# Optimization experiments

Hardware: AMD Instinct MI355X
Metric: run time of the kernel (lower is better)

The kernel has to match this reference:

```python
import jax, jax.numpy as jnp
import numpy as np
import math

DIM = 1024
NUM_HEADS = 16
HEAD_DIM = DIM // NUM_HEADS
ROPE_BASE = 10000.0


def _rope_cos_sin(seq_len, head_dim, dtype):
    inv_freq = 1.0 / (ROPE_BASE ** (jnp.arange(0, head_dim, 2, dtype=jnp.float32) / head_dim))
    t = jnp.arange(seq_len, dtype=jnp.float32)
    freqs = jnp.einsum('i,j->ij', t, inv_freq)          # (S, head_dim/2)
    emb = jnp.concatenate([freqs, freqs], axis=-1)      # (S, head_dim)
    return jnp.cos(emb).astype(dtype), jnp.sin(emb).astype(dtype)


def _rotate_half(x):
    x1, x2 = jnp.split(x, 2, axis=-1)
    return jnp.concatenate([-x2, x1], axis=-1)


def setup_inputs() -> dict:
    key = jax.random.key(0)
    kx, kq, kk, kv, ko = jax.random.split(key, 5)
    B, S = 4, 2048
    scale = 1.0 / math.sqrt(DIM)
    x = jax.random.normal(kx, (B, S, DIM), dtype=jnp.float32)
    Wq = jax.random.normal(kq, (DIM, DIM), dtype=jnp.float32) * scale
    Wk = jax.random.normal(kk, (DIM, DIM), dtype=jnp.float32) * scale
    Wv = jax.random.normal(kv, (DIM, DIM), dtype=jnp.float32) * scale
    Wo = jax.random.normal(ko, (DIM, DIM), dtype=jnp.float32) * scale
    mask = jnp.tril(jnp.ones((S, S), dtype=jnp.int32))  # causal mask
    return {"x": x, "Wq": Wq, "Wk": Wk, "Wv": Wv, "Wo": Wo, "mask": mask}


def reference(x, Wq, Wk, Wv, Wo, mask):
    B, S, _ = x.shape
    # projections (nn.Linear: y = x @ W.T)
    def split_heads(t):
        return t.reshape(B, S, NUM_HEADS, HEAD_DIM).transpose(0, 2, 1, 3)  # (B,H,S,D)
    q = split_heads(x @ Wq.T)
    k = split_heads(x @ Wk.T)
    v = split_heads(x @ Wv.T)
    # RoPE
    cos, sin = _rope_cos_sin(S, HEAD_DIM, x.dtype)      # (S, D)
    cos = cos[None, None]; sin = sin[None, None]
    q = q * cos + _rotate_half(q) * sin
    k = k * cos + _rotate_half(k) * sin
    # attention
    scores = jnp.einsum('bhsd,bhtd->bhst', q, k) / math.sqrt(HEAD_DIM)
    neg_inf = jnp.asarray(-jnp.inf, dtype=scores.dtype)
    scores = jnp.where(mask[None, None] == 0, neg_inf, scores)
    attn = jax.nn.softmax(scores, axis=-1)
    out = jnp.einsum('bhst,bhtd->bhsd', attn, v)        # (B,H,S,D)
    out = out.transpose(0, 2, 1, 3).reshape(B, S, DIM)
    return out @ Wo.T
```

## Files before the change

kernel.cpp:

```cpp
#include <hip/hip_runtime.h>
#include <hip/hip_bf16.h>

#define BDIM 1024
#define NH 16
#define HD 64
#define BB 4
#define SS 2048
#define MTOT (BB*SS)
#define NT (SS/64)

typedef __bf16 bf16x8 __attribute__((ext_vector_type(8)));
typedef float f32x4 __attribute__((ext_vector_type(4)));

__device__ __forceinline__ unsigned short f2b(float f){
    __bf16 h = (__bf16)f;
    return __builtin_bit_cast(unsigned short, h);
}

__device__ __forceinline__ void ld16(const unsigned short* g, unsigned short* l){
    __builtin_amdgcn_global_load_lds(
        (const __attribute__((address_space(1))) unsigned int*)(const void*)g,
        (__attribute__((address_space(3))) unsigned int*)(void*)l, 16, 0, 0);
}

__global__ void setup_all(const float* __restrict__ x,
                          const float* __restrict__ Wq, const float* __restrict__ Wk,
                          const float* __restrict__ Wv, const float* __restrict__ Wo,
                          unsigned short* __restrict__ xb,
                          unsigned short* __restrict__ oq, unsigned short* __restrict__ ok,
                          unsigned short* __restrict__ ov, unsigned short* __restrict__ oo,
                          float2* __restrict__ rt){
    const int bid = blockIdx.x;
    const int tid = threadIdx.x;
    if (bid < 8192){
        int i = bid * 256 + tid;
        float4 v = ((const float4*)x)[i];
        ushort4 o;
        o.x = f2b(v.x); o.y = f2b(v.y); o.z = f2b(v.z); o.w = f2b(v.w);
        ((ushort4*)xb)[i] = o;
    } else if (bid < 12288){
        int idx = bid - 8192;
        int which = idx >> 10;
        const float* in = (which == 0) ? Wq : (which == 1) ? Wk : (which == 2) ? Wv : Wo;
        unsigned short* out = (which == 0) ? oq : (which == 1) ? ok : (which == 2) ? ov : oo;
        int i = (idx & 1023) * 256 + tid;
        float4 v = ((const float4*)in)[i];
        ushort4 o;
        o.x = f2b(v.x); o.y = f2b(v.y); o.z = f2b(v.z); o.w = f2b(v.w);
        ((ushort4*)out)[i] = o;
    } else {
        int i = (bid - 12288) * 256 + tid;
        int s = i >> 5, d = i & 31;
        float theta = (float)s * exp2f(-0.41524101186092029f * (float)d);
        float sn, c;
        sincosf(theta, &sn, &c);
        rt[i] = make_float2(c, sn);
    }
}

__device__ __forceinline__ void gemm_mainloop(
    const unsigned short* __restrict__ A,
    const unsigned short* __restrict__ Bw,
    unsigned short* At, unsigned short* Bt,
    f32x4 acc[4][4], int m0, int n0)
{
    const int tid  = threadIdx.x;
    const int lane = tid & 63;
    const int wave = tid >> 6;
    const int wr = wave >> 1, wc = wave & 1;
    const int lh = lane >> 4, ll = lane & 15;
    const int K = 1024;

    for (int k0 = 0; k0 < K; k0 += 64){
        #pragma unroll
        for (int c = 0; c < 4; ++c){
            int g   = c*256 + tid;
            int row = g >> 3;
            int off = (g & 7) * 8;
            int base = (c*256 + wave*64) * 8;
            ld16(A  + (size_t)(m0+row)*K + k0 + off, At + base);
            ld16(Bw + (size_t)(n0+row)*K + k0 + off, Bt + base);
        }
        __syncthreads();
        #pragma unroll
        for (int ks = 0; ks < 2; ++ks){
            bf16x8 af[4], bfr[4];
            #pragma unroll
            for (int i = 0; i < 4; ++i)
                af[i] = *(const bf16x8*)(At + (wr*64 + i*16 + ll)*64 + ks*32 + lh*8);
            #pragma unroll
            for (int j = 0; j < 4; ++j)
                bfr[j] = *(const bf16x8*)(Bt + (wc*64 + j*16 + ll)*64 + ks*32 + lh*8);
            #pragma unroll
            for (int i = 0; i < 4; ++i)
                #pragma unroll
                for (int j = 0; j < 4; ++j)
                    acc[i][j] = __builtin_amdgcn_mfma_f32_16x16x32_bf16(af[i], bfr[j], acc[i][j], 0, 0, 0);
        }
        __syncthreads();
    }
}

#define TILE_US 4096

__global__ __launch_bounds__(256, 4) void gemm_qkv(
    const unsigned short* __restrict__ Xb,
    const unsigned short* __restrict__ Wq,
    const unsigned short* __restrict__ Wk,
    const unsigned short* __restrict__ Wv,
    const float2* __restrict__ Rt,
    unsigned short* __restrict__ Qt,
    unsigned short* __restrict__ Kt,
    unsigned short* __restrict__ VTt)
{
    __shared__ alignas(16) unsigned short At[128*64];
    __shared__ alignas(16) unsigned short Bt[128*64];
    const int z = blockIdx.z;
    const unsigned short* Bw = (z == 0) ? Wq : (z == 1 ? Wk : Wv);
    const int m0 = blockIdx.y * 128, n0 = blockIdx.x * 128;
    f32x4 acc[4][4] = {};
    gemm_mainloop(Xb, Bw, At, Bt, acc, m0, n0);

    const int lane = threadIdx.x & 63;
    const int wave = threadIdx.x >> 6;
    const int wr = wave >> 1, wc = wave & 1;
    const int lh = lane >> 4, ll = lane & 15;
    const int h  = blockIdx.x*2 + wc;
    const int b  = m0 >> 11;
    const int bh = b*NH + h;

    if (z < 2){
        const float qs = (z == 0) ? 0.125f * 1.44269504f : 1.0f;
        unsigned short* C = (z == 0) ? Qt : Kt;
        #pragma unroll
        for (int i = 0; i < 4; ++i)
            #pragma unroll
            for (int r = 0; r < 4; ++r){
                int m = m0 + wr*64 + i*16 + lh*4 + r;
                int s = m & (SS-1);
                int kt = s >> 6;
                const float2* rowcs = Rt + (s << 5);
                size_t fb = ((size_t)(bh*NT + kt)*8 + i)*512 + (size_t)(lh*4 + r)*8;
                #pragma unroll
                for (int jl = 0; jl < 2; ++jl){
                    int d_lo = jl*16 + ll;
                    float2 cs = rowcs[d_lo];
                    float a_lo = acc[i][jl][r], a_hi = acc[i][jl+2][r];
                    float y_lo = (a_lo*cs.x - a_hi*cs.y) * qs;
                    float y_hi = (a_hi*cs.x + a_lo*cs.y) * qs;
                    size_t off = fb + (size_t)(jl*2 + (ll>>3))*128 + (ll&7);
                    C[off]        = f2b(y_lo);
                    C[off + 2048] = f2b(y_hi);
                }
            }
    } else {
        const int s0 = (m0 & (SS-1)) + wr*64;
        const int kt = s0 >> 6;
        #pragma unroll
        for (int i = 0; i < 4; ++i)
            #pragma unroll
            for (int j = 0; j < 4; ++j){
                unsigned short tmp[4];
                #pragma unroll
                for (int r = 0; r < 4; ++r)
                    tmp[r] = f2b(acc[i][j][r]);
                size_t off = ((size_t)(bh*NT + kt)*8 + (i>>1)*4 + j)*512
                           + (size_t)(((i&1)*2 + (lh>>1))*16 + ll)*8 + (lh&1)*4;
                *(uint2*)(VTt + off) = *(const uint2*)tmp;
            }
    }
}

__global__ __launch_bounds__(256, 4) void gemm_out(
    const unsigned short* __restrict__ Ab,
    const unsigned short* __restrict__ Wo,
    float* __restrict__ Cout)
{
    __shared__ alignas(16) unsigned short At[128*64];
    __shared__ alignas(16) unsigned short Bt[128*64];
    const int m0 = blockIdx.y * 128, n0 = blockIdx.x * 128;
    f32x4 acc[4][4] = {};
    gemm_mainloop(Ab, Wo, At, Bt, acc, m0, n0);

    const int lane = threadIdx.x & 63;
    const int wave = threadIdx.x >> 6;
    const int wr = wave >> 1, wc = wave & 1;
    const int lh = lane >> 4, ll = lane & 15;
    #pragma unroll
    for (int i = 0; i < 4; ++i)
        #pragma unroll
        for (int j = 0; j < 4; ++j)
            #pragma unroll
            for (int r = 0; r < 4; ++r){
                int m = m0 + wr*64 + i*16 + lh*4 + r;
                int n = n0 + wc*64 + j*16 + ll;
                Cout[(size_t)m*BDIM + n] = acc[i][j][r];
            }
}

__device__ __forceinline__ void attn_tile(
    const bf16x8 qf[2], bool diag, int ws, int lane, int lh, int ll,
    const unsigned short* Ksh, const unsigned short* Vsh, unsigned short* Prow,
    float li[4], f32x4 o[4])
{
    f32x4 sc[4] = {};
    #pragma unroll
    for (int ks = 0; ks < 2; ++ks)
        #pragma unroll
        for (int j = 0; j < 4; ++j){
            bf16x8 bfr = *(const bf16x8*)(Ksh + (ks*4 + j)*512 + lane*8);
            sc[j] = __builtin_amdgcn_mfma_f32_16x16x32_bf16(qf[ks], bfr, sc[j], 0, 0, 0);
        }
    if (diag){
        #pragma unroll
        for (int j = 0; j < 4; ++j){
            int key = j*16 + ll;
            #pragma unroll
            for (int r = 0; r < 4; ++r){
                int qrow = ws*16 + lh*4 + r;
                if (key > qrow) sc[j][r] = -1e30f;
            }
        }
    }
    #pragma unroll
    for (int j = 0; j < 4; ++j)
        #pragma unroll
        for (int r = 0; r < 4; ++r)
            sc[j][r] = exp2f(sc[j][r] - 28.0f);
    #pragma unroll
    for (int r = 0; r < 4; ++r)
        li[r] += (sc[0][r] + sc[1][r]) + (sc[2][r] + sc[3][r]);
    #pragma unroll
    for (int j = 0; j < 4; ++j)
        #pragma unroll
        for (int r = 0; r < 4; ++r)
            Prow[(lh*4 + r)*72 + j*16 + ll] = f2b(sc[j][r]);
    #pragma unroll
    for (int ks = 0; ks < 2; ++ks){
        bf16x8 pf = *(const bf16x8*)(Prow + ll*72 + ks*32 + lh*8);
        #pragma unroll
        for (int t = 0; t < 4; ++t){
            bf16x8 vf = *(const bf16x8*)(Vsh + (ks*4 + t)*512 + lane*8);
            o[t] = __builtin_amdgcn_mfma_f32_16x16x32_bf16(pf, vf, o[t], 0, 0, 0);
        }
    }
}

__device__ __forceinline__ void store_o(
    unsigned short* S, const f32x4 o[4], const float li[4],
    int lane, int lh, int ll, int q0w, int b, int h,
    unsigned short* __restrict__ Obuf)
{
    #pragma unroll
    for (int r = 0; r < 4; ++r){
        float inv = 1.0f / li[r];
        #pragma unroll
        for (int t = 0; t < 4; ++t)
            S[(lh*4 + r)*72 + t*16 + ll] = f2b(o[t][r] * inv);
    }
    int row = lane >> 2, c4 = (lane & 3) * 8;
    size_t rb = ((size_t)(b*SS + q0w + row))*BDIM + h*HD;
    *(uint4*)(Obuf + rb + c4)      = *(uint4*)(S + row*72 + c4);
    *(uint4*)(Obuf + rb + 32 + c4) = *(uint4*)(S + row*72 + 32 + c4);
}

__global__ __launch_bounds__(512, 4) void attn_kernel(
    const unsigned short* __restrict__ Qt,
    const unsigned short* __restrict__ Kt,
    const unsigned short* __restrict__ VTt,
    unsigned short* __restrict__ Obuf)
{
    __shared__ alignas(16) unsigned short Ksh[2][TILE_US];
    __shared__ alignas(16) unsigned short Vsh[2][TILE_US];
    __shared__ alignas(16) unsigned short Psh[8][16*72];

    const int tid  = threadIdx.x;
    const int lane = tid & 63;
    const int wave = tid >> 6;
    const int grp  = wave >> 2;
    const int ws   = wave & 3;
    const int lh = lane >> 4, ll = lane & 15;
    const int bx = blockIdx.x;
    const int bh = blockIdx.y;

    const int tS = (grp == 0) ? bx        : 15 - bx;
    const int tL = (grp == 0) ? NT-1 - bx : 16 + bx;
    const int ktMax = NT-1 - bx;

    const unsigned short* Qhf = Qt  + (size_t)bh * NT * TILE_US;
    const unsigned short* Khf = Kt  + (size_t)bh * NT * TILE_US;
    const unsigned short* Vhf = VTt + (size_t)bh * NT * TILE_US;

    bf16x8 qfS[2], qfL[2];
    #pragma unroll
    for (int ks = 0; ks < 2; ++ks){
        qfS[ks] = *(const bf16x8*)(Qhf + (size_t)(tS*8 + ks*4 + ws)*512 + lane*8);
        qfL[ks] = *(const bf16x8*)(Qhf + (size_t)(tL*8 + ks*4 + ws)*512 + lane*8);
    }

    f32x4 oS[4] = {}, oL[4] = {};
    float liS[4] = {0.f,0.f,0.f,0.f}, liL[4] = {0.f,0.f,0.f,0.f};

    const int tb = tid * 8;

    {
        uint4 k0 = *(const uint4*)(Khf + tb);
        uint4 v0 = *(const uint4*)(Vhf + tb);
        *(uint4*)(&Ksh[0][0] + tb) = k0;
        *(uint4*)(&Vsh[0][0] + tb) = v0;
    }
    __syncthreads();

    int cur = 0;
    for (int kt = 0; kt <= ktMax; ++kt){
        uint4 kr, vr;
        if (kt < ktMax){
            size_t nb = (size_t)(kt + 1) * TILE_US + tb;
            kr = *(const uint4*)(Khf + nb);
            vr = *(const uint4*)(Vhf + nb);
        }
        if (kt <= tL)
            attn_tile(qfL, kt == tL, ws, lane, lh, ll, &Ksh[cur][0], &Vsh[cur][0], Psh[wave], liL, oL);
        if (kt <= tS)
            attn_tile(qfS, kt == tS, ws, lane, lh, ll, &Ksh[cur][0], &Vsh[cur][0], Psh[wave], liS, oS);
        if (kt < ktMax){
            *(uint4*)(&Ksh[cur^1][0] + tb) = kr;
            *(uint4*)(&Vsh[cur^1][0] + tb) = vr;
        }
        __syncthreads();
        cur ^= 1;
    }

    #pragma unroll
    for (int r = 0; r < 4; ++r){
        float sS = liS[r], sL = liL[r];
        #pragma unroll
        for (int x = 1; x < 16; x <<= 1){
            sS += __shfl_xor(sS, x);
            sL += __shfl_xor(sL, x);
        }
        liS[r] = sS; liL[r] = sL;
    }

    int b = bh >> 4, h = bh & 15;
    store_o(Psh[wave], oS, liS, lane, lh, ll, tS*64 + ws*16, b, h, Obuf);
    store_o(Psh[wave], oL, liL, lane, lh, ll, tL*64 + ws*16, b, h, Obuf);
}

extern "C" void kernel_launch(void* const* d_in, const int* in_sizes, int n_in,
                              void* d_out, int out_size, void* d_ws, size_t ws_size,
                              hipStream_t stream) {
    const float* x  = (const float*)d_in[0];
    const float* Wq = (const float*)d_in[1];
    const float* Wk = (const float*)d_in[2];
    const float* Wv = (const float*)d_in[3];
    const float* Wo = (const float*)d_in[4];

    char* w = (char*)d_ws;
    unsigned short* xb  = (unsigned short*)(w);
    unsigned short* wqb = (unsigned short*)(w + (16u  << 20));
    unsigned short* wkb = (unsigned short*)(w + (18u  << 20));
    unsigned short* wvb = (unsigned short*)(w + (20u  << 20));
    unsigned short* wob = (unsigned short*)(w + (22u  << 20));
    unsigned short* Qt  = (unsigned short*)(w + (24u  << 20));
    unsigned short* Kt  = (unsigned short*)(w + (40u  << 20));
    unsigned short* VTt = (unsigned short*)(w + (56u  << 20));
    unsigned short* Ob  = (unsigned short*)(w + (72u  << 20));
    float2*         Rt  = (float2*)(w + (88u << 20));

    setup_all<<<12544, 256, 0, stream>>>(x, Wq, Wk, Wv, Wo, xb, wqb, wkb, wvb, wob, Rt);

    gemm_qkv<<<dim3(8, 64, 3), 256, 0, stream>>>(xb, wqb, wkb, wvb, Rt, Qt, Kt, VTt);
    attn_kernel<<<dim3(8, 64), 512, 0, stream>>>(Qt, Kt, VTt, Ob);
    gemm_out<<<dim3(8, 64), 256, 0, stream>>>(Ob, wob, (float*)d_out);
}
```

Measured before the change: 283.9 us.

## Compute transposed scores and build P fragments in registers via permlane swaps

The QK^T MFMA now computes S^T by swapping operands, so each lane holds scores for a single query row. The P operand for the PV MFMA is then built directly in registers with packed bf16 conversion and permlane16/32 swaps, instead of being written to and re-read from a per-wave LDS buffer. This removes the LDS round trip and scalar bf16 stores from the inner attention loop, and it simplifies the row-sum reduction to two shuffles at the end. The cost is inline asm that relies on gfx950 permlane instructions and a correct fragment mapping.

```diff
diff --git a/kernel.cpp b/kernel.cpp
--- a/kernel.cpp
+++ b/kernel.cpp
@@ -15,6 +15,12 @@
 __device__ __forceinline__ unsigned short f2b(float f){
     __bf16 h = (__bf16)f;
     return __builtin_bit_cast(unsigned short, h);
+}
+
+__device__ __forceinline__ unsigned cvtpk(float lo, float hi){
+    unsigned u;
+    asm("v_cvt_pk_bf16_f32 %0, %1, %2" : "=v"(u) : "v"(lo), "v"(hi));
+    return u;
 }
 
 __device__ __forceinline__ void ld16(const unsigned short* g, unsigned short* l){
@@ -200,44 +206,47 @@
 
 __device__ __forceinline__ void attn_tile(
     const bf16x8 qf[2], bool diag, int ws, int lane, int lh, int ll,
-    const unsigned short* Ksh, const unsigned short* Vsh, unsigned short* Prow,
-    float li[4], f32x4 o[4])
+    const unsigned short* Ksh, const unsigned short* Vsh,
+    float& li, f32x4 o[4])
 {
     f32x4 sc[4] = {};
     #pragma unroll
     for (int ks = 0; ks < 2; ++ks)
         #pragma unroll
         for (int j = 0; j < 4; ++j){
-            bf16x8 bfr = *(const bf16x8*)(Ksh + (ks*4 + j)*512 + lane*8);
-            sc[j] = __builtin_amdgcn_mfma_f32_16x16x32_bf16(qf[ks], bfr, sc[j], 0, 0, 0);
+            bf16x8 kfr = *(const bf16x8*)(Ksh + (ks*4 + j)*512 + lane*8);
+            sc[j] = __builtin_amdgcn_mfma_f32_16x16x32_bf16(kfr, qf[ks], sc[j], 0, 0, 0);
         }
     if (diag){
-        #pragma unroll
-        for (int j = 0; j < 4; ++j){
-            int key = j*16 + ll;
-            #pragma unroll
-            for (int r = 0; r < 4; ++r){
-                int qrow = ws*16 + lh*4 + r;
-                if (key > qrow) sc[j][r] = -1e30f;
-            }
-        }
+        int qrow = ws*16 + ll;
+        #pragma unroll
+        for (int j = 0; j < 4; ++j)
+            #pragma unroll
+            for (int r = 0; r < 4; ++r)
+                if (j*16 + lh*4 + r > qrow) sc[j][r] = -1e30f;
     }
     #pragma unroll
     for (int j = 0; j < 4; ++j)
         #pragma unroll
         for (int r = 0; r < 4; ++r)
             sc[j][r] = exp2f(sc[j][r] - 28.0f);
-    #pragma unroll
-    for (int r = 0; r < 4; ++r)
-        li[r] += (sc[0][r] + sc[1][r]) + (sc[2][r] + sc[3][r]);
+    float s = 0.f;
     #pragma unroll
     for (int j = 0; j < 4; ++j)
-        #pragma unroll
-        for (int r = 0; r < 4; ++r)
-            Prow[(lh*4 + r)*72 + j*16 + ll] = f2b(sc[j][r]);
+        s += (sc[j][0] + sc[j][1]) + (sc[j][2] + sc[j][3]);
+    li += s;
     #pragma unroll
     for (int ks = 0; ks < 2; ++ks){
-        bf16x8 pf = *(const bf16x8*)(Prow + ll*72 + ks*32 + lh*8);
+        unsigned a = cvtpk(sc[2*ks][0],   sc[2*ks][1]);
+        unsigned b = cvtpk(sc[2*ks+1][0], sc[2*ks+1][1]);
+        unsigned c = cvtpk(sc[2*ks][2],   sc[2*ks][3]);
+        unsigned d = cvtpk(sc[2*ks+1][2], sc[2*ks+1][3]);
+        asm("v_permlane32_swap_b32 %0, %1" : "+v"(a), "+v"(b));
+        asm("v_permlane16_swap_b32 %0, %1" : "+v"(a), "+v"(b));
+        asm("v_permlane32_swap_b32 %0, %1" : "+v"(c), "+v"(d));
+        asm("v_permlane16_swap_b32 %0, %1" : "+v"(c), "+v"(d));
+        uint4 uu = make_uint4(a, c, b, d);
+        bf16x8 pf = __builtin_bit_cast(bf16x8, uu);
         #pragma unroll
         for (int t = 0; t < 4; ++t){
             bf16x8 vf = *(const bf16x8*)(Vsh + (ks*4 + t)*512 + lane*8);
@@ -299,7 +308,7 @@
     }
 
     f32x4 oS[4] = {}, oL[4] = {};
-    float liS[4] = {0.f,0.f,0.f,0.f}, liL[4] = {0.f,0.f,0.f,0.f};
+    float liS = 0.f, liL = 0.f;
 
     const int tb = tid * 8;
 
@@ -320,9 +329,9 @@
             vr = *(const uint4*)(Vhf + nb);
         }
         if (kt <= tL)
-            attn_tile(qfL, kt == tL, ws, lane, lh, ll, &Ksh[cur][0], &Vsh[cur][0], Psh[wave], liL, oL);
+            attn_tile(qfL, kt == tL, ws, lane, lh, ll, &Ksh[cur][0], &Vsh[cur][0], liL, oL);
         if (kt <= tS)
-            attn_tile(qfS, kt == tS, ws, lane, lh, ll, &Ksh[cur][0], &Vsh[cur][0], Psh[wave], liS, oS);
+            attn_tile(qfS, kt == tS, ws, lane, lh, ll, &Ksh[cur][0], &Vsh[cur][0], liS, oS);
         if (kt < ktMax){
             *(uint4*)(&Ksh[cur^1][0] + tb) = kr;
             *(uint4*)(&Vsh[cur^1][0] + tb) = vr;
@@ -331,20 +340,18 @@
         cur ^= 1;
     }
 
+    liS += __shfl_xor(liS, 16); liS += __shfl_xor(liS, 32);
+    liL += __shfl_xor(liL, 16); liL += __shfl_xor(liL, 32);
+    float livS[4], livL[4];
     #pragma unroll
     for (int r = 0; r < 4; ++r){
-        float sS = liS[r], sL = liL[r];
-        #pragma unroll
-        for (int x = 1; x < 16; x <<= 1){
-            sS += __shfl_xor(sS, x);
-            sL += __shfl_xor(sL, x);
-        }
-        liS[r] = sS; liL[r] = sL;
+        livS[r] = __shfl(liS, lh*4 + r);
+        livL[r] = __shfl(liL, lh*4 + r);
     }
 
     int b = bh >> 4, h = bh & 15;
-    store_o(Psh[wave], oS, liS, lane, lh, ll, tS*64 + ws*16, b, h, Obuf);
-    store_o(Psh[wave], oL, liL, lane, lh, ll, tL*64 + ws*16, b, h, Obuf);
+    store_o(Psh[wave], oS, livS, lane, lh, ll, tS*64 + ws*16, b, h, Obuf);
+    store_o(Psh[wave], oL, livL, lane, lh, ll, tL*64 + ws*16, b, h, Obuf);
 }
 
 extern "C" void kernel_launch(void* const* d_in, const int* in_sizes, int n_in,
```

Result: faster. 275.1 us (-3.1%).
